# Performance work log

Measured on AMD Instinct MI355X. Metric: run time of the kernel, lower is better.

## Reference

```python
import jax, jax.numpy as jnp
import numpy as np

TOP_K = 4
NORM_TOPK_PROB = False  # Qwen2-MoE default

def setup_inputs() -> dict:
    key = jax.random.key(0)
    ks = jax.random.split(key, 10)
    B, S, D = 1, 2048, 2048
    E, F, FS = 8, 1408, 5632
    s = 0.02
    return {
        "hidden_states": jax.random.normal(ks[0], (B, S, D), jnp.float32),
        "gate_w": jax.random.normal(ks[1], (E, D), jnp.float32) * s,          # router Linear weight [E, D]
        "Wg": jax.random.normal(ks[2], (E, D, F), jnp.float32) * s,           # expert gate_proj
        "Wu": jax.random.normal(ks[3], (E, D, F), jnp.float32) * s,           # expert up_proj
        "Wd": jax.random.normal(ks[4], (E, F, D), jnp.float32) * s,           # expert down_proj
        "Wsg": jax.random.normal(ks[5], (D, FS), jnp.float32) * s,            # shared gate_proj
        "Wsu": jax.random.normal(ks[6], (D, FS), jnp.float32) * s,            # shared up_proj
        "Wsd": jax.random.normal(ks[7], (FS, D), jnp.float32) * s,            # shared down_proj
        "shared_gate_w": jax.random.normal(ks[8], (D, 1), jnp.float32) * s,   # shared_expert_gate Linear(D,1)
    }

def reference(hidden_states, gate_w, Wg, Wu, Wd, Wsg, Wsu, Wsd, shared_gate_w):
    B, S, D = hidden_states.shape
    x = hidden_states.reshape(-1, D)                       # [T, D]
    T = x.shape[0]
    router_logits = x @ gate_w.T                           # [T, E]
    probs = jax.nn.softmax(router_logits.astype(jnp.float32), axis=-1)
    top_vals, top_idx = jax.lax.top_k(probs, TOP_K)        # [T, K]
    if NORM_TOPK_PROB:
        top_vals = top_vals / jnp.sum(top_vals, axis=-1, keepdims=True)
    # dense routing-weight matrix: zero for unselected experts (same math as masked naive loop)
    w = jnp.zeros_like(probs).at[jnp.arange(T)[:, None], top_idx].set(top_vals)
    w = w.astype(x.dtype)                                  # [T, E]
    # per-expert SiLU-gated MLP, computed densely over all experts
    h = jax.nn.silu(jnp.einsum('td,edf->etf', x, Wg)) * jnp.einsum('td,edf->etf', x, Wu)  # [E, T, F]
    expert_out = jnp.einsum('etf,efd->etd', h, Wd)         # [E, T, D]
    moe_out = jnp.einsum('etd,te->td', expert_out, w)      # [T, D]
    # shared expert with sigmoid gate
    shared = (jax.nn.silu(x @ Wsg) * (x @ Wsu)) @ Wsd      # [T, D]
    shared = jax.nn.sigmoid(x @ shared_gate_w) * shared    # [T,1] * [T,D]
    out = (moe_out + shared).reshape(B, S, D)
    return out, router_logits
```

## Files before the change

kernel.cpp:

```cpp
#include <hip/hip_runtime.h>
#include <hip/hip_bf16.h>

typedef __attribute__((ext_vector_type(8))) __bf16 bf16x8;
typedef __attribute__((ext_vector_type(4))) float f32x4;

#define TKN 2048
#define DMODEL 2048
#define NEXP 8
#define FEXP 1408
#define FSH 5632

__device__ __forceinline__ unsigned short f2bf(float f) {
  unsigned u = __float_as_uint(f);
  u += 0x7FFFu + ((u >> 16) & 1u);
  return (unsigned short)(u >> 16);
}
__device__ __forceinline__ unsigned pk2(float a, float b) {
  return (unsigned)f2bf(a) | ((unsigned)f2bf(b) << 16);
}

__device__ __forceinline__ void gll16(const void* g, void* l) {
  __builtin_amdgcn_global_load_lds(
      (const __attribute__((address_space(1))) unsigned*)g,
      (__attribute__((address_space(3))) unsigned*)l, 16, 0, 0);
}

enum { EPI_GU = 0, EPI_DOWN = 1, EPI_SDOWN = 2 };

__global__ __launch_bounds__(256)
void router_k(const float* __restrict__ x, const float* __restrict__ gw,
              const float* __restrict__ sgw, float* __restrict__ logits,
              float* __restrict__ sig, int* __restrict__ cnt,
              int* __restrict__ tokl, float* __restrict__ wls)
{
  const int wv = threadIdx.x >> 6, lane = threadIdx.x & 63;
  const int t = blockIdx.x * 4 + wv;
  const float* xr = x + (long)t * DMODEL;
  float xv[32];
#pragma unroll
  for (int j = 0; j < 32; j++) xv[j] = xr[lane + (j << 6)];

  float lg[8];
#pragma unroll
  for (int e = 0; e < 8; e++) {
    const float* gr = gw + (long)e * DMODEL;
    float acc = 0.f;
#pragma unroll
    for (int j = 0; j < 32; j++) acc += xv[j] * gr[lane + (j << 6)];
#pragma unroll
    for (int s = 1; s < 64; s <<= 1) acc += __shfl_xor(acc, s, 64);
    lg[e] = acc;
  }
  float sgacc = 0.f;
#pragma unroll
  for (int j = 0; j < 32; j++) sgacc += xv[j] * sgw[lane + (j << 6)];
#pragma unroll
  for (int s = 1; s < 64; s <<= 1) sgacc += __shfl_xor(sgacc, s, 64);

  if (lane == 0) {
    float mx = lg[0];
#pragma unroll
    for (int e = 1; e < 8; e++) mx = fmaxf(mx, lg[e]);
    float p[8], se = 0.f;
#pragma unroll
    for (int e = 0; e < 8; e++) { p[e] = expf(lg[e] - mx); se += p[e]; }
    float inv = 1.f / se;
#pragma unroll
    for (int e = 0; e < 8; e++) { p[e] *= inv; logits[t * 8 + e] = lg[e]; }
    sig[t] = 1.f / (1.f + expf(-sgacc));
#pragma unroll
    for (int k = 0; k < 4; k++) {
      int bi = 0; float bv = p[0];
#pragma unroll
      for (int e = 1; e < 8; e++) if (p[e] > bv) { bv = p[e]; bi = e; }
      p[bi] = -1.f;
      int pos = atomicAdd(&cnt[bi], 1);
      tokl[bi * TKN + pos] = t;
      wls[bi * TKN + pos] = bv;
    }
  }
}

__global__ void scan_k(const int* __restrict__ cnt, int* __restrict__ offs) {
  if (threadIdx.x == 0) {
    int s = 0;
    for (int e = 0; e < 8; e++) { offs[e] = s; s += cnt[e]; }
    offs[8] = s;
  }
}

__global__ __launch_bounds__(256)
void cvt_x_k(const float* __restrict__ x, char* __restrict__ xbf)
{
  long id = (long)blockIdx.x * 256 + threadIdx.x;
  int row = id >> 8, u = id & 255, kt = u >> 2, j = u & 3;
  const float* p = x + (long)row * 2048 + kt * 32 + j * 4;
  float4 a = *(const float4*)p;
  float4 b = *(const float4*)(p + 16);
  uint4 o;
  o.x = pk2(a.x, a.y); o.y = pk2(a.z, a.w);
  o.z = pk2(b.x, b.y); o.w = pk2(b.z, b.w);
  *(uint4*)(xbf + id * 16) = o;
}

__global__ __launch_bounds__(256)
void cvt_w_k(const float* __restrict__ W, long sB, int N,
             char* __restrict__ panel, long panStride)
{
  const int ct = blockIdx.x, kt = blockIdx.y, e = blockIdx.z, KT = gridDim.y;
  const float* Wp = W + (long)e * sB + (long)(kt * 32) * N + ct * 128;
  __shared__ float t[32][128];
  const int r = threadIdx.x >> 3, q = threadIdx.x & 7;
  const float* rp = Wp + (long)r * N + q * 16;
  float4 f0 = *(const float4*)(rp + 0);
  float4 f1 = *(const float4*)(rp + 4);
  float4 f2 = *(const float4*)(rp + 8);
  float4 f3 = *(const float4*)(rp + 12);
  *(float4*)&t[r][q * 16 + 0]  = f0;
  *(float4*)&t[r][q * 16 + 4]  = f1;
  *(float4*)&t[r][q * 16 + 8]  = f2;
  *(float4*)&t[r][q * 16 + 12] = f3;
  __syncthreads();
  char* outp = panel + e * panStride + ((long)ct * KT + kt) * 8192;
#pragma unroll
  for (int uu = 0; uu < 2; uu++) {
    int u = threadIdx.x + uu * 256;
    int c = u >> 2;
    int g = (u & 3) ^ ((c >> 1) & 3);
    uint4 o;
    o.x = pk2(t[g * 4 + 0][c], t[g * 4 + 1][c]);
    o.y = pk2(t[g * 4 + 2][c], t[g * 4 + 3][c]);
    o.z = pk2(t[16 + g * 4 + 0][c], t[16 + g * 4 + 1][c]);
    o.w = pk2(t[16 + g * 4 + 2][c], t[16 + g * 4 + 3][c]);
    *(uint4*)(outp + u * 16) = o;
  }
}

__global__ __launch_bounds__(256)
void cvt_gu_k(const float* __restrict__ Wg, const float* __restrict__ Wu,
              long sB, int N, char* __restrict__ panel, long panStride)
{
  const int ct = blockIdx.x, kt = blockIdx.y, e = blockIdx.z, KT = gridDim.y;
  __shared__ float t[32][128];
  const int r = threadIdx.x >> 3, q = threadIdx.x & 7;
  const float* src = ((q >> 1) & 1) ? Wu : Wg;
  const int scol = ct * 64 + ((q >> 2) << 5) + ((q & 1) << 4);
  const float* rp = src + (long)e * sB + (long)(kt * 32 + r) * N + scol;
  float4 f0 = *(const float4*)(rp + 0);
  float4 f1 = *(const float4*)(rp + 4);
  float4 f2 = *(const float4*)(rp + 8);
  float4 f3 = *(const float4*)(rp + 12);
  *(float4*)&t[r][q * 16 + 0]  = f0;
  *(float4*)&t[r][q * 16 + 4]  = f1;
  *(float4*)&t[r][q * 16 + 8]  = f2;
  *(float4*)&t[r][q * 16 + 12] = f3;
  __syncthreads();
  char* outp = panel + e * panStride + ((long)ct * KT + kt) * 8192;
#pragma unroll
  for (int uu = 0; uu < 2; uu++) {
    int u = threadIdx.x + uu * 256;
    int c = u >> 2;
    int g = (u & 3) ^ ((c >> 1) & 3);
    uint4 o;
    o.x = pk2(t[g * 4 + 0][c], t[g * 4 + 1][c]);
    o.y = pk2(t[g * 4 + 2][c], t[g * 4 + 3][c]);
    o.z = pk2(t[16 + g * 4 + 0][c], t[16 + g * 4 + 1][c]);
    o.w = pk2(t[16 + g * 4 + 2][c], t[16 + g * 4 + 3][c]);
    *(uint4*)(outp + u * 16) = o;
  }
}

template<int EPI, bool EXPERT, int KSPLIT>
__global__ __launch_bounds__(256, 3)
void gemm2_k(const char* __restrict__ Abf, long strA,
             const char* __restrict__ Bp, long sBpan, int KTtot, int NCT,
             void* __restrict__ O, int ldKo,
             const int* __restrict__ cnt, const int* __restrict__ offs,
             const int* __restrict__ tokl, const float* __restrict__ wls,
             const float* __restrict__ sig)
{
  const int tid = threadIdx.x, lane = tid & 63, w = tid >> 6;
  const int wg = blockIdx.x;

  int e = 0, rt, ct, kc = 0, M = TKN;
  if (EXPERT) {
    e = wg & 7; int q = wg >> 3; rt = q & 15; ct = q >> 4;
    M = cnt[e];
    if (rt * 128 >= M) return;
  } else {
    rt = wg & 15; int q = wg >> 4; ct = q % NCT; kc = q / NCT;
  }
  const int KT = KTtot / KSPLIT;
  const int kt0 = kc * KT;
  const int obase = EXPERT ? offs[e] : 0;

  __shared__ int s_tok[128];
  __shared__ float s_w[128];
  __shared__ alignas(16) char Ab[3][8192];
  __shared__ alignas(16) char Bb[3][8192];

  if (EXPERT) {
    if (tid < 128) {
      int r = rt * 128 + tid;
      int rc = (r < M) ? r : (M - 1);
      s_tok[tid] = tokl[e * TKN + rc];
      if (EPI == EPI_DOWN) s_w[tid] = (r < M) ? wls[e * TKN + r] : 0.f;
    }
    __syncthreads();
  }

  const int lrow0 = w * 32 + (lane >> 2);
  const int lrow1 = lrow0 + 16;
  auto rowbyte = [&](int rl) -> long {
    long gr;
    if (EPI == EPI_DOWN) { int r = rt * 128 + rl; gr = obase + ((r < M) ? r : (M - 1)); }
    else if (EXPERT)     { gr = s_tok[rl]; }
    else                 { gr = rt * 128 + rl; }
    return gr * strA;
  };
  const int au0 = (lane & 3) ^ ((lrow0 >> 1) & 3);
  const int au1 = (lane & 3) ^ ((lrow1 >> 1) & 3);
  const char* gA0 = Abf + rowbyte(lrow0) + (long)kt0 * 64 + au0 * 16;
  const char* gA1 = Abf + rowbyte(lrow1) + (long)kt0 * 64 + au1 * 16;
  const long bbase = (EXPERT ? (long)e * sBpan : 0) + ((long)ct * KTtot + kt0) * 8192
                     + w * 2048 + (long)lane * 16;
  const char* gB = Bp + bbase;

  auto stage = [&](int bf, int kt) {
    long ao = (long)kt * 64, bo = (long)kt * 8192;
    gll16(gA0 + ao, &Ab[bf][w * 2048]);
    gll16(gA1 + ao, &Ab[bf][w * 2048 + 1024]);
    gll16(gB + bo, &Bb[bf][w * 2048]);
    gll16(gB + bo + 1024, &Bb[bf][w * 2048 + 1024]);
  };

  const int wm = w >> 1, wn = w & 1, g = lane >> 4, l15 = lane & 15;
  int raOff[4], rbOff[4];
#pragma unroll
  for (int m = 0; m < 4; m++) {
    int row = wm * 64 + m * 16 + l15;
    raOff[m] = row * 64 + ((g ^ ((row >> 1) & 3)) << 4);
  }
#pragma unroll
  for (int n = 0; n < 4; n++) {
    int col = wn * 64 + n * 16 + l15;
    rbOff[n] = col * 64 + ((g ^ ((col >> 1) & 3)) << 4);
  }

  f32x4 acc[4][4] = {};

  stage(0, 0);
  stage(1, 1);

  int rd = 0;
#pragma unroll 1
  for (int kt = 0; kt < KT; ++kt) {
    if (kt + 1 < KT) asm volatile("s_waitcnt vmcnt(4)" ::: "memory");
    else             asm volatile("s_waitcnt vmcnt(0)" ::: "memory");
    __builtin_amdgcn_s_barrier();
    __builtin_amdgcn_sched_barrier(0);

    bf16x8 av[4], bv[4];
#pragma unroll
    for (int m = 0; m < 4; m++) av[m] = *(const bf16x8*)&Ab[rd][raOff[m]];
#pragma unroll
    for (int n = 0; n < 4; n++) bv[n] = *(const bf16x8*)&Bb[rd][rbOff[n]];

    int wr = rd + 2; if (wr >= 3) wr -= 3;
    if (kt + 2 < KT) stage(wr, kt + 2);

    __builtin_amdgcn_s_setprio(1);
#pragma unroll
    for (int m = 0; m < 4; m++)
#pragma unroll
      for (int n = 0; n < 4; n++)
        acc[m][n] = __builtin_amdgcn_mfma_f32_16x16x32_bf16(av[m], bv[n], acc[m][n], 0, 0, 0);
    __builtin_amdgcn_s_setprio(0);
    __builtin_amdgcn_sched_barrier(0);
    rd = (rd == 2) ? 0 : rd + 1;
  }

  if constexpr (EPI == EPI_GU) {
#pragma unroll
    for (int m = 0; m < 4; m++) {
#pragma unroll
      for (int n = 0; n < 2; n++) {
        int lc = ct * 64 + wn * 32 + n * 16 + l15;
        f32x4 ga = acc[m][n];
        f32x4 ua = acc[m][n + 2];
#pragma unroll
        for (int q = 0; q < 4; q++) {
          int rl = wm * 64 + m * 16 + (g << 2) + q;
          int grow = rt * 128 + rl;
          if (!EXPERT || grow < M) {
            float gv = ga[q];
            float hv = (gv / (1.f + __expf(-gv))) * ua[q];
            long byteoff = (long)(obase + grow) * ((long)ldKo * 64)
                         + (lc >> 5) * 64 + ((lc >> 2) & 3) * 16
                         + ((lc & 16) >> 1) + (lc & 3) * 2;
            *(unsigned short*)((char*)O + byteoff) = f2bf(hv);
          }
        }
      }
    }
  } else {
#pragma unroll
    for (int m = 0; m < 4; m++) {
#pragma unroll
      for (int n = 0; n < 4; n++) {
        int col = ct * 128 + wn * 64 + n * 16 + l15;
        f32x4 a = acc[m][n];
#pragma unroll
        for (int q = 0; q < 4; q++) {
          int rl = wm * 64 + m * 16 + (g << 2) + q;
          int grow = rt * 128 + rl;
          float v = a[q];
          if constexpr (EPI == EPI_DOWN) {
            if (grow < M)
              atomicAdd((float*)O + (long)s_tok[rl] * DMODEL + col, s_w[rl] * v);
          } else {
            atomicAdd((float*)O + (long)grow * DMODEL + col, sig[grow] * v);
          }
        }
      }
    }
  }
}

__device__ __forceinline__ void block_sync_fb() {
  __builtin_amdgcn_sched_barrier(0);
  asm volatile("s_waitcnt lgkmcnt(0)" ::: "memory");
  __builtin_amdgcn_s_barrier();
  __builtin_amdgcn_sched_barrier(0);
}

template<int EPI, bool EXPERT, int KSPLIT>
__global__ __launch_bounds__(256, 2)
void gemm_fb_k(const float* __restrict__ A, int lda,
               const float* __restrict__ B, const float* __restrict__ B2,
               long sB, int ldb, int Ktot,
               float* __restrict__ O, int ldo,
               const int* __restrict__ cnt, const int* __restrict__ offs,
               const int* __restrict__ tokl, const float* __restrict__ wls,
               const float* __restrict__ sig)
{
  constexpr bool FUSED = (EPI == EPI_GU);
  const int tid = threadIdx.x;
  const int lane = tid & 63;

  int e = 0, rt, kc = 0, M = TKN;
  if (EXPERT) {
    e = blockIdx.y >> 4; rt = blockIdx.y & 15;
    M = cnt[e];
    if (rt * 128 >= M) return;
  } else {
    rt = blockIdx.y & 15; kc = blockIdx.y >> 4;
  }
  const int K = Ktot / KSPLIT;
  const int koff = kc * K;
  const int colblk = blockIdx.x * 128;
  const float* Bp  = B + (EXPERT ? (long)e * sB : 0);
  const float* Bp2 = FUSED ? (B2 + (EXPERT ? (long)e * sB : 0)) : nullptr;
  const int obase = EXPERT ? offs[e] : 0;

  __shared__ alignas(16) unsigned char Ab[8192];
  __shared__ alignas(16) unsigned char Bb[8192];
  __shared__ alignas(16) unsigned char Bb2[FUSED ? 8192 : 16];
  __shared__ int s_tok[128];
  __shared__ float s_w[128];

  if (EXPERT && tid < 128) {
    int r = rt * 128 + tid;
    int rc = (r < M) ? r : (M - 1);
    s_tok[tid] = tokl[e * TKN + rc];
    if (EPI == EPI_DOWN) s_w[tid] = (r < M) ? wls[e * TKN + r] : 0.f;
  }
  if (EXPERT) __syncthreads();

  const int arowl = tid >> 1;
  const int ahalf = tid & 1;
  long arow;
  if (EPI == EPI_DOWN) {
    int r = rt * 128 + arowl;
    arow = (long)obase + ((r < M) ? r : (M - 1));
  } else if (EXPERT) {
    arow = s_tok[arowl];
  } else {
    arow = rt * 128 + arowl;
  }
  const float* aptr = A + arow * (long)lda + koff + ahalf * 16;
  int wa[4];
#pragma unroll
  for (int j = 0; j < 4; j++)
    wa[j] = arowl * 64 + ((j ^ ((arowl ^ (arowl >> 3)) & 3)) << 4) + ahalf * 8;

  const int kg = tid >> 5, ng = tid & 31;
  const float* bptr  = Bp + (long)(koff + kg * 4) * ldb + colblk + ng * 4;
  const float* bptr2 = FUSED ? (Bp2 + (long)(koff + kg * 4) * ldb + colblk + ng * 4) : nullptr;
  int wb[4];
#pragma unroll
  for (int i = 0; i < 4; i++) {
    int c = ng * 4 + i;
    wb[i] = c * 64 + ((((kg & 3) ^ ((c ^ (c >> 3)) & 3))) << 4) + (kg >> 2) * 8;
  }

  const int wid = tid >> 6, wm = wid >> 1, wn = wid & 1;
  const int g = lane >> 4, l15 = lane & 15;
  int ra[4], rb[4];
#pragma unroll
  for (int m = 0; m < 4; m++) {
    int r = wm * 64 + m * 16 + l15;
    ra[m] = r * 64 + ((g ^ ((r ^ (r >> 3)) & 3)) << 4);
  }
#pragma unroll
  for (int n = 0; n < 4; n++) {
    int c = wn * 64 + n * 16 + l15;
    rb[n] = c * 64 + ((g ^ ((c ^ (c >> 3)) & 3)) << 4);
  }

  f32x4 acc[4][4] = {};
  f32x4 acc2[4][4] = {};

  const int KT = K >> 5;
  float4 ta0[4], tb0[4], tc0[4], ta1[4], tb1[4], tc1[4];

  auto load_tile = [&](float4* ra_, float4* rb_, float4* rc_, int kt) {
    const float4* a4 = reinterpret_cast<const float4*>(aptr + kt * 32);
    ra_[0] = a4[0]; ra_[1] = a4[1]; ra_[2] = a4[2]; ra_[3] = a4[3];
    const float* bb = bptr + (long)kt * 32 * ldb;
    rb_[0] = *reinterpret_cast<const float4*>(bb);
    rb_[1] = *reinterpret_cast<const float4*>(bb + ldb);
    rb_[2] = *reinterpret_cast<const float4*>(bb + 2 * ldb);
    rb_[3] = *reinterpret_cast<const float4*>(bb + 3 * ldb);
    if (FUSED) {
      const float* cc = bptr2 + (long)kt * 32 * ldb;
      rc_[0] = *reinterpret_cast<const float4*>(cc);
      rc_[1] = *reinterpret_cast<const float4*>(cc + ldb);
      rc_[2] = *reinterpret_cast<const float4*>(cc + 2 * ldb);
      rc_[3] = *reinterpret_cast<const float4*>(cc + 3 * ldb);
    }
  };

  auto store_tile = [&](const float4* ra_, const float4* rb_, const float4* rc_) {
#pragma unroll
    for (int j = 0; j < 4; j++)
      *reinterpret_cast<uint2*>(Ab + wa[j]) =
          make_uint2(pk2(ra_[j].x, ra_[j].y), pk2(ra_[j].z, ra_[j].w));
    *reinterpret_cast<uint2*>(Bb + wb[0]) = make_uint2(pk2(rb_[0].x, rb_[1].x), pk2(rb_[2].x, rb_[3].x));
    *reinterpret_cast<uint2*>(Bb + wb[1]) = make_uint2(pk2(rb_[0].y, rb_[1].y), pk2(rb_[2].y, rb_[3].y));
    *reinterpret_cast<uint2*>(Bb + wb[2]) = make_uint2(pk2(rb_[0].z, rb_[1].z), pk2(rb_[2].z, rb_[3].z));
    *reinterpret_cast<uint2*>(Bb + wb[3]) = make_uint2(pk2(rb_[0].w, rb_[1].w), pk2(rb_[2].w, rb_[3].w));
    if (FUSED) {
      *reinterpret_cast<uint2*>(Bb2 + wb[0]) = make_uint2(pk2(rc_[0].x, rc_[1].x), pk2(rc_[2].x, rc_[3].x));
      *reinterpret_cast<uint2*>(Bb2 + wb[1]) = make_uint2(pk2(rc_[0].y, rc_[1].y), pk2(rc_[2].y, rc_[3].y));
      *reinterpret_cast<uint2*>(Bb2 + wb[2]) = make_uint2(pk2(rc_[0].z, rc_[1].z), pk2(rc_[2].z, rc_[3].z));
      *reinterpret_cast<uint2*>(Bb2 + wb[3]) = make_uint2(pk2(rc_[0].w, rc_[1].w), pk2(rc_[2].w, rc_[3].w));
    }
  };

  auto mfma_step = [&]() {
    bf16x8 av[4], bvg[4], bvu[4];
#pragma unroll
    for (int m = 0; m < 4; m++) av[m] = *reinterpret_cast<const bf16x8*>(Ab + ra[m]);
#pragma unroll
    for (int n = 0; n < 4; n++) {
      bvg[n] = *reinterpret_cast<const bf16x8*>(Bb + rb[n]);
      if (FUSED) bvu[n] = *reinterpret_cast<const bf16x8*>(Bb2 + rb[n]);
    }
#pragma unroll
    for (int m = 0; m < 4; m++)
#pragma unroll
      for (int n = 0; n < 4; n++) {
        acc[m][n] = __builtin_amdgcn_mfma_f32_16x16x32_bf16(av[m], bvg[n], acc[m][n], 0, 0, 0);
        if (FUSED)
          acc2[m][n] = __builtin_amdgcn_mfma_f32_16x16x32_bf16(av[m], bvu[n], acc2[m][n], 0, 0, 0);
      }
  };

  load_tile(ta0, tb0, tc0, 0);
#pragma unroll 1
  for (int kt = 0; kt < KT; kt += 2) {
    load_tile(ta1, tb1, tc1, kt + 1);
    store_tile(ta0, tb0, tc0);
    block_sync_fb();
    mfma_step();
    block_sync_fb();
    int k2 = (kt + 2 < KT) ? kt + 2 : 0;
    load_tile(ta0, tb0, tc0, k2);
    store_tile(ta1, tb1, tc1);
    block_sync_fb();
    mfma_step();
    block_sync_fb();
  }

#pragma unroll
  for (int m = 0; m < 4; m++) {
#pragma unroll
    for (int n = 0; n < 4; n++) {
      int col = colblk + wn * 64 + n * 16 + l15;
      f32x4 a = acc[m][n];
      f32x4 a2 = acc2[m][n];
#pragma unroll
      for (int q = 0; q < 4; q++) {
        int rl = wm * 64 + m * 16 + (g << 2) + q;
        int grow = rt * 128 + rl;
        float v = a[q];
        if (EPI == EPI_GU) {
          if (!EXPERT || grow < M) {
            float hv = (v / (1.f + __expf(-v))) * a2[q];
            O[(long)(obase + grow) * ldo + col] = hv;
          }
        } else if (EPI == EPI_DOWN) {
          if (grow < M)
            atomicAdd(&O[(long)s_tok[rl] * ldo + col], s_w[rl] * v);
        } else {
          atomicAdd(&O[(long)grow * ldo + col], sig[grow] * v);
        }
      }
    }
  }
}

extern "C" void kernel_launch(void* const* d_in, const int* in_sizes, int n_in,
                              void* d_out, int out_size, void* d_ws, size_t ws_size,
                              hipStream_t stream)
{
  (void)in_sizes; (void)n_in; (void)out_size;
  const float* x   = (const float*)d_in[0];
  const float* gw  = (const float*)d_in[1];
  const float* Wg  = (const float*)d_in[2];
  const float* Wu  = (const float*)d_in[3];
  const float* Wd  = (const float*)d_in[4];
  const float* Wsg = (const float*)d_in[5];
  const float* Wsu = (const float*)d_in[6];
  const float* Wsd = (const float*)d_in[7];
  const float* sgw = (const float*)d_in[8];

  float* out    = (float*)d_out;
  float* logits = out + (long)TKN * DMODEL;

  char* w    = (char*)d_ws;
  int*  cnt  = (int*)w;
  int*  offs = (int*)(w + 64);
  float* sig = (float*)(w + 1024);
  int*  tokl = (int*)(w + 16384);
  float* wls = (float*)(w + 81920);

  hipMemsetAsync(out, 0, (size_t)TKN * DMODEL * 4, stream);
  hipMemsetAsync(cnt, 0, 64, stream);

  router_k<<<dim3(TKN / 4), 256, 0, stream>>>(x, gw, sgw, logits, sig, cnt, tokl, wls);
  scan_k<<<1, 64, 0, stream>>>(cnt, offs);

  const size_t NEED = 241172480ull;
  if (ws_size >= NEED) {
    char* xbf     = w + 262144;
    char* h       = w + 8650752;
    char* panGUex = w + 33554432;
    char* panWd   = w + 125829120;
    char* panGUsh = w + 171966464;
    char* panWsd  = w + 218103808;
    const long sPanGU = 11534336;
    const long sPanWd = 5767168;

    cvt_x_k<<<dim3(2048), 256, 0, stream>>>(x, xbf);
    cvt_gu_k<<<dim3(22, 64, 8), 256, 0, stream>>>(Wg, Wu, (long)DMODEL * FEXP, FEXP, panGUex, sPanGU);
    cvt_w_k<<<dim3(16, 44, 8), 256, 0, stream>>>(Wd, (long)FEXP * DMODEL, DMODEL, panWd, sPanWd);
    cvt_gu_k<<<dim3(88, 64, 1), 256, 0, stream>>>(Wsg, Wsu, 0, FSH, panGUsh, 0);
    cvt_w_k<<<dim3(16, 176, 1), 256, 0, stream>>>(Wsd, 0, DMODEL, panWsd, 0);

    gemm2_k<EPI_GU, true, 1><<<dim3(8 * 16 * 22), 256, 0, stream>>>(
        xbf, 4096, panGUex, sPanGU, 64, 22, h, 44, cnt, offs, tokl, wls, nullptr);
    gemm2_k<EPI_DOWN, true, 1><<<dim3(8 * 16 * 16), 256, 0, stream>>>(
        h, 2816, panWd, sPanWd, 44, 16, out, 0, cnt, offs, tokl, wls, nullptr);
    gemm2_k<EPI_GU, false, 1><<<dim3(16 * 88), 256, 0, stream>>>(
        xbf, 4096, panGUsh, 0, 64, 88, h, 176, nullptr, nullptr, nullptr, nullptr, nullptr);
    gemm2_k<EPI_SDOWN, false, 4><<<dim3(16 * 16 * 4), 256, 0, stream>>>(
        h, 11264, panWsd, 0, 176, 16, out, 0, nullptr, nullptr, nullptr, nullptr, sig);
  } else {
    float* h = (float*)(w + (1 << 20));
    gemm_fb_k<EPI_GU, true, 1><<<dim3(FEXP / 128, 128), 256, 0, stream>>>(
        x, DMODEL, Wg, Wu, (long)DMODEL * FEXP, FEXP, DMODEL, h, FEXP, cnt, offs, tokl, wls, nullptr);
    gemm_fb_k<EPI_DOWN, true, 1><<<dim3(DMODEL / 128, 128), 256, 0, stream>>>(
        h, FEXP, Wd, nullptr, (long)FEXP * DMODEL, DMODEL, FEXP, out, DMODEL, cnt, offs, tokl, wls, nullptr);
    gemm_fb_k<EPI_GU, false, 1><<<dim3(FSH / 128, TKN / 128), 256, 0, stream>>>(
        x, DMODEL, Wsg, Wsu, 0, FSH, DMODEL, h, FSH, nullptr, nullptr, nullptr, nullptr, nullptr);
    gemm_fb_k<EPI_SDOWN, false, 4><<<dim3(DMODEL / 128, (TKN / 128) * 4), 256, 0, stream>>>(
        h, FSH, Wsd, nullptr, 0, DMODEL, FSH, out, DMODEL, nullptr, nullptr, nullptr, nullptr, sig);
  }
}
```

Measured before the change: 680.1 us.

## Replace triple-buffered LDS pipeline with single buffer and raise occupancy

Removes the three-stage global-to-LDS prefetch pipeline in the GEMM kernel and uses one LDS buffer, synchronised with two __syncthreads per k-step. It also raises the launch-bounds occupancy hint from 3 to 4 blocks per CU. The aim is to rely on more resident waves instead of software pipelining to hide memory latency. The risk is that loads are no longer overlapped with MFMA work inside a block, so each iteration stalls on global load latency. The change also drops the priority hints. Correctness depends on __syncthreads draining the asynchronous global_load_lds transfers before LDS is read.

```diff
diff --git a/kernel.cpp b/kernel.cpp
--- a/kernel.cpp
+++ b/kernel.cpp
@@ -171,7 +171,7 @@
 }
 
 template<int EPI, bool EXPERT, int KSPLIT>
-__global__ __launch_bounds__(256, 3)
+__global__ __launch_bounds__(256, 4)
 void gemm2_k(const char* __restrict__ Abf, long strA,
              const char* __restrict__ Bp, long sBpan, int KTtot, int NCT,
              void* __restrict__ O, int ldKo,
@@ -196,8 +196,8 @@
 
   __shared__ int s_tok[128];
   __shared__ float s_w[128];
-  __shared__ alignas(16) char Ab[3][8192];
-  __shared__ alignas(16) char Bb[3][8192];
+  __shared__ alignas(16) char Ab[8192];
+  __shared__ alignas(16) char Bb[8192];
 
   if (EXPERT) {
     if (tid < 128) {
@@ -226,14 +226,6 @@
                      + w * 2048 + (long)lane * 16;
   const char* gB = Bp + bbase;
 
-  auto stage = [&](int bf, int kt) {
-    long ao = (long)kt * 64, bo = (long)kt * 8192;
-    gll16(gA0 + ao, &Ab[bf][w * 2048]);
-    gll16(gA1 + ao, &Ab[bf][w * 2048 + 1024]);
-    gll16(gB + bo, &Bb[bf][w * 2048]);
-    gll16(gB + bo + 1024, &Bb[bf][w * 2048 + 1024]);
-  };
-
   const int wm = w >> 1, wn = w & 1, g = lane >> 4, l15 = lane & 15;
   int raOff[4], rbOff[4];
 #pragma unroll
@@ -249,35 +241,26 @@
 
   f32x4 acc[4][4] = {};
 
-  stage(0, 0);
-  stage(1, 1);
-
-  int rd = 0;
 #pragma unroll 1
   for (int kt = 0; kt < KT; ++kt) {
-    if (kt + 1 < KT) asm volatile("s_waitcnt vmcnt(4)" ::: "memory");
-    else             asm volatile("s_waitcnt vmcnt(0)" ::: "memory");
-    __builtin_amdgcn_s_barrier();
-    __builtin_amdgcn_sched_barrier(0);
+    long ao = (long)kt * 64, bo = (long)kt * 8192;
+    gll16(gA0 + ao, &Ab[w * 2048]);
+    gll16(gA1 + ao, &Ab[w * 2048 + 1024]);
+    gll16(gB + bo, &Bb[w * 2048]);
+    gll16(gB + bo + 1024, &Bb[w * 2048 + 1024]);
+    __syncthreads();
 
     bf16x8 av[4], bv[4];
 #pragma unroll
-    for (int m = 0; m < 4; m++) av[m] = *(const bf16x8*)&Ab[rd][raOff[m]];
-#pragma unroll
-    for (int n = 0; n < 4; n++) bv[n] = *(const bf16x8*)&Bb[rd][rbOff[n]];
-
-    int wr = rd + 2; if (wr >= 3) wr -= 3;
-    if (kt + 2 < KT) stage(wr, kt + 2);
-
-    __builtin_amdgcn_s_setprio(1);
+    for (int m = 0; m < 4; m++) av[m] = *(const bf16x8*)&Ab[raOff[m]];
+#pragma unroll
+    for (int n = 0; n < 4; n++) bv[n] = *(const bf16x8*)&Bb[rbOff[n]];
 #pragma unroll
     for (int m = 0; m < 4; m++)
 #pragma unroll
       for (int n = 0; n < 4; n++)
         acc[m][n] = __builtin_amdgcn_mfma_f32_16x16x32_bf16(av[m], bv[n], acc[m][n], 0, 0, 0);
-    __builtin_amdgcn_s_setprio(0);
-    __builtin_amdgcn_sched_barrier(0);
-    rd = (rd == 2) ? 0 : rd + 1;
+    __syncthreads();
   }
 
   if constexpr (EPI == EPI_GU) {
```

Result: slower. 742.9 us (+9.2%).
